# Performance work log

Hardware: AMD Instinct MI355X
Metric: run time of the kernel (lower is better)

## Reference

```python
import jax, jax.numpy as jnp
import numpy as np

DIM = 1024
H = 16
DH = DIM // H
LN_EPS = 1e-5


def _linear_params(key, din, dout):
    kw, kb = jax.random.split(key)
    bound = 1.0 / np.sqrt(din)
    W = jax.random.uniform(kw, (din, dout), jnp.float32, -bound, bound)
    b = jax.random.uniform(kb, (dout,), jnp.float32, -bound, bound)
    return W, b


def setup_inputs() -> dict:
    key = jax.random.key(0)
    ks = jax.random.split(key, 10)
    inp = {
        "Q": jax.random.normal(ks[0], (8, 512, DIM), jnp.float32),
        "K1": jax.random.normal(ks[1], (8, 1024, DIM), jnp.float32),
        "K2": jax.random.normal(ks[2], (8, 1024, DIM), jnp.float32),
    }
    for name, k in zip(["q", "k1", "k2", "v1", "v2", "o"], ks[3:9]):
        W, b = _linear_params(k, DIM, DIM)
        inp["W" + name] = W
        inp["b" + name] = b
    inp["g0"] = jnp.ones((DIM,), jnp.float32)
    inp["beta0"] = jnp.zeros((DIM,), jnp.float32)
    inp["g1"] = jnp.ones((DIM,), jnp.float32)
    inp["beta1"] = jnp.zeros((DIM,), jnp.float32)
    return inp


def _layernorm(x, g, b):
    m = jnp.mean(x, axis=-1, keepdims=True)
    v = jnp.mean(jnp.square(x - m), axis=-1, keepdims=True)
    return (x - m) * jax.lax.rsqrt(v + LN_EPS) * g + b


def _split_heads(x):
    # torch.cat(x.split(dh, 2), dim=0): [B,N,D] -> [H*B, N, dh], head-major on axis 0
    B, N, _ = x.shape
    return x.reshape(B, N, H, DH).transpose(2, 0, 1, 3).reshape(H * B, N, DH)


def _merge_heads(x, B):
    # inverse: torch.cat(out.split(B, 0), 2)
    _, N, _ = x.shape
    return x.reshape(H, B, N, DH).transpose(1, 2, 0, 3).reshape(B, N, DIM)


def reference(Q, K1, K2, Wq, bq, Wk1, bk1, Wk2, bk2, Wv1, bv1, Wv2, bv2, Wo, bo, g0, beta0, g1, beta1):
    B = Q.shape[0]
    Qp = Q @ Wq + bq
    # NOTE: faithful to source — V is computed from the ALREADY key-projected K_dict
    K1p = K1 @ Wk1 + bk1
    K2p = K2 @ Wk2 + bk2
    V1p = K1p @ Wv1 + bv1
    V2p = K2p @ Wv2 + bv2
    Q_ = _split_heads(Qp)                                   # [H*B, Nq, dh]
    K_ = jnp.concatenate([_split_heads(K1p), _split_heads(K2p)], axis=1)  # [H*B, Nk, dh]
    V_ = jnp.concatenate([_split_heads(V1p), _split_heads(V2p)], axis=1)
    scores = jnp.einsum("bqd,bkd->bqk", Q_, K_) / np.sqrt(DIM).astype(np.float32)
    # NOTE: faithful to source — softmax over the QUERY axis (dim=1)
    A = jax.nn.softmax(scores, axis=1)
    out = Q_ + jnp.einsum("bqk,bkd->bqd", A, V_)
    out = _merge_heads(out, B)                              # [B, Nq, DIM]
    out = _layernorm(out, g0, beta0)
    out = out + jax.nn.relu(out @ Wo + bo)
    out = _layernorm(out, g1, beta1)
    return out
```

## Files before the change

### kernel.cpp

```cpp
#include <hip/hip_runtime.h>
#include <math.h>

typedef __attribute__((ext_vector_type(8))) _Float16 half8v;
typedef __attribute__((ext_vector_type(4))) _Float16 half4v;
typedef __attribute__((ext_vector_type(4))) float f32x4;

__device__ __forceinline__ void gload16(const void* g, void* l) {
  __builtin_amdgcn_global_load_lds(
      (const __attribute__((address_space(1))) void*)g,
      (__attribute__((address_space(3))) void*)l, 16, 0, 0);
}

struct WP { const float* src; _Float16* dst; };
struct WPArgs { WP w[6]; };

__global__ __launch_bounds__(256)
void wprep_kernel(WPArgs args) {
  __shared__ float tile[32][33];
  const WP wp = args.w[blockIdx.z];
  const int t  = threadIdx.x;
  const int r  = t >> 3;
  const int c  = (t & 7) * 4;
  const int n0 = blockIdx.x * 32;
  const int k0 = blockIdx.y * 32;
  float4 v = *(const float4*)(wp.src + (size_t)(k0 + r) * 1024 + n0 + c);
  tile[r][c] = v.x; tile[r][c + 1] = v.y; tile[r][c + 2] = v.z; tile[r][c + 3] = v.w;
  __syncthreads();
  half4v h;
  #pragma unroll
  for (int i = 0; i < 4; ++i) h[i] = (_Float16)tile[c + i][r];
  *(half4v*)(wp.dst + (size_t)(n0 + r) * 1024 + k0 + c) = h;
}

__global__ __launch_bounds__(256)
void aconv_kernel(const float* __restrict__ in, _Float16* __restrict__ out, int n4) {
  int i = blockIdx.x * 256 + threadIdx.x;
  if (i >= n4) return;
  float4 v = ((const float4*)in)[i];
  half4v o;
  o[0] = (_Float16)v.x; o[1] = (_Float16)v.y; o[2] = (_Float16)v.z; o[3] = (_Float16)v.w;
  ((half4v*)out)[i] = o;
}

template<int MODE>
__global__ __launch_bounds__(256)
void gemm_fp16(const _Float16* __restrict__ A, const _Float16* __restrict__ B,
               const float* __restrict__ bias, const _Float16* __restrict__ X,
               _Float16* __restrict__ C, float* __restrict__ Cf,
               _Float16* __restrict__ Vt, int NM) {
  __shared__ _Float16 smem[16384];
  _Float16* const sA = smem;
  _Float16* const sB = smem + 8192;
  const int t    = threadIdx.x;
  const int bid  = blockIdx.x;
  const int xcd  = bid & 7;
  const int li   = bid >> 3;
  const int m    = xcd * (NM >> 3) + (li >> 3);
  const int n    = li & 7;
  const int bm   = m * 128;
  const int bn   = n * 128;
  const int lane = t & 63;
  const int w    = t >> 6;
  const int wr   = (w >> 1) * 64;
  const int wc   = (w & 1) * 64;
  const int lm   = lane & 15;
  const int lq   = lane >> 4;

  f32x4 acc[4][4];
  #pragma unroll
  for (int i = 0; i < 4; ++i)
    #pragma unroll
    for (int j = 0; j < 4; ++j) { f32x4 z = {0.f, 0.f, 0.f, 0.f}; acc[i][j] = z; }

  for (int k0 = 0; k0 < 1024; k0 += 64) {
    __syncthreads();
    #pragma unroll
    for (int i = 0; i < 4; ++i) {
      const int T    = w * 4 + i;
      const int kq   = T >> 1;
      const int row  = (T & 1) * 64 + lane;
      gload16(A + (size_t)(bm + row) * 1024 + k0 + kq * 8, &sA[(T * 64 + lane) * 8]);
      gload16(B + (size_t)(bn + row) * 1024 + k0 + kq * 8, &sB[(T * 64 + lane) * 8]);
    }
    __syncthreads();

    #pragma unroll
    for (int kk = 0; kk < 2; ++kk) {
      half8v af[4], bf[4];
      #pragma unroll
      for (int mi = 0; mi < 4; ++mi)
        af[mi] = *(const half8v*)&sA[((kk * 4 + lq) * 128 + wr + mi * 16 + lm) * 8];
      #pragma unroll
      for (int ni = 0; ni < 4; ++ni)
        bf[ni] = *(const half8v*)&sB[((kk * 4 + lq) * 128 + wc + ni * 16 + lm) * 8];
      #pragma unroll
      for (int mi = 0; mi < 4; ++mi)
        #pragma unroll
        for (int ni = 0; ni < 4; ++ni)
          acc[mi][ni] = __builtin_amdgcn_mfma_f32_16x16x32_f16(af[mi], bf[ni], acc[mi][ni], 0, 0, 0);
    }
  }

  float bv[4];
  #pragma unroll
  for (int ni = 0; ni < 4; ++ni) bv[ni] = bias[bn + wc + ni * 16 + lm];

  if (MODE == 1) {
    #pragma unroll
    for (int mi = 0; mi < 4; ++mi)
      #pragma unroll
      for (int ni = 0; ni < 4; ++ni) {
        const int col = bn + wc + ni * 16 + lm;
        #pragma unroll
        for (int j = 0; j < 4; ++j) {
          const int row = bm + wr + mi * 16 + lq * 4 + j;
          const size_t idx = (size_t)row * 1024 + col;
          Cf[idx] = (float)X[idx] + fmaxf(acc[mi][ni][j] + bv[ni], 0.f);
        }
      }
    return;
  }

  __syncthreads();
  #pragma unroll
  for (int mi = 0; mi < 4; ++mi)
    #pragma unroll
    for (int ni = 0; ni < 4; ++ni) {
      const int cc = wc + ni * 16 + lm;
      #pragma unroll
      for (int j = 0; j < 4; ++j) {
        const int rr = wr + mi * 16 + lq * 4 + j;
        const _Float16 v = (_Float16)(acc[mi][ni][j] + bv[ni]);
        if (MODE == 0) smem[rr * 128 + cc] = v;
        else           smem[cc * 128 + rr] = v;
      }
    }
  __syncthreads();
  const int r16 = t >> 4;
  const int c8  = (t & 15) * 8;
  #pragma unroll
  for (int p = 0; p < 8; ++p) {
    const int row = p * 16 + r16;
    half8v vv = *(const half8v*)&smem[row * 128 + c8];
    if (MODE == 0) *(half8v*)(C + (size_t)(bm + row) * 1024 + bn + c8) = vv;
    else           *(half8v*)(Vt + (size_t)(bn + row) * 8192 + bm + c8) = vv;
  }
}

__global__ __launch_bounds__(1024, 4)
void attn_mfma(const _Float16* __restrict__ Qp,
               const _Float16* __restrict__ K1p, const _Float16* __restrict__ K2p,
               const _Float16* __restrict__ VT1, const _Float16* __restrict__ VT2,
               float* __restrict__ Opart) {
  __shared__ _Float16 sK[2][2048];
  __shared__ _Float16 sV[2][2560];
  __shared__ _Float16 sP[20480];
  __shared__ float sZ[16][32];

  const int t    = threadIdx.x;
  const int lane = t & 63;
  const int w    = t >> 6;
  const int lm   = lane & 15;
  const int lq   = lane >> 4;
  const int hb   = blockIdx.x;
  const int ks   = blockIdx.y;
  const int h    = hb >> 3;
  const int b    = hb & 7;
  const int qw   = w * 32;
  const _Float16* __restrict__ K  = ks ? K2p : K1p;
  const _Float16* __restrict__ VT = ks ? VT2 : VT1;

  half8v qf[2][2];
  #pragma unroll
  for (int mi = 0; mi < 2; ++mi)
    #pragma unroll
    for (int dh = 0; dh < 2; ++dh)
      qf[mi][dh] = *(const half8v*)(Qp + (size_t)(b * 512 + qw + mi * 16 + lm) * 1024
                                       + h * 64 + dh * 32 + lq * 8);

  f32x4 o[2][4];
  #pragma unroll
  for (int i = 0; i < 2; ++i)
    #pragma unroll
    for (int j = 0; j < 4; ++j) { f32x4 z = {0.f, 0.f, 0.f, 0.f}; o[i][j] = z; }

  const int ku = t & 255;
  const int sd = ku & 31;
  const int sc = ku >> 5;
  const int vd = ku & 63;
  const int vc = (ku >> 6) & 3;
  _Float16* sPw = sP + w * 1280;

  half8v rk, rv;
  #define ISSUE_LOADS(K0)                                                                  \
    if (t < 256)      rk = *(const half8v*)(K + (size_t)(b * 1024 + (K0) + sd) * 1024 + h * 64 + sc * 8); \
    else if (t < 512) rv = *(const half8v*)(VT + (size_t)(h * 64 + vd) * 8192 + b * 1024 + (K0) + vc * 8);

  ISSUE_LOADS(0)

  for (int kt = 0; kt < 32; ++kt) {
    const int c = kt & 1;
    if (t < 256)      *(half8v*)&sK[c][(sc * 32 + sd) * 8] = rk;
    else if (t < 512) *(half8v*)&sV[c][vd * 40 + vc * 8] = rv;
    if (kt + 1 < 32) { ISSUE_LOADS((kt + 1) * 32) }
    __syncthreads();

    f32x4 s[2][2];
    #pragma unroll
    for (int i = 0; i < 2; ++i)
      #pragma unroll
      for (int j = 0; j < 2; ++j) { f32x4 z = {0.f, 0.f, 0.f, 0.f}; s[i][j] = z; }
    __builtin_amdgcn_s_setprio(1);
    #pragma unroll
    for (int dh = 0; dh < 2; ++dh) {
      half8v kb[2];
      #pragma unroll
      for (int fi = 0; fi < 2; ++fi)
        kb[fi] = *(const half8v*)&sK[c][((dh * 4 + lq) * 32 + fi * 16 + lm) * 8];
      #pragma unroll
      for (int mi = 0; mi < 2; ++mi)
        #pragma unroll
        for (int fi = 0; fi < 2; ++fi)
          s[mi][fi] = __builtin_amdgcn_mfma_f32_16x16x32_f16(qf[mi][dh], kb[fi], s[mi][fi], 0, 0, 0);
    }
    __builtin_amdgcn_s_setprio(0);

    float zp[2] = {0.f, 0.f};
    #pragma unroll
    for (int mi = 0; mi < 2; ++mi)
      #pragma unroll
      for (int fi = 0; fi < 2; ++fi)
        #pragma unroll
        for (int j = 0; j < 4; ++j) {
          float p = __expf(s[mi][fi][j] * 0.03125f);
          s[mi][fi][j] = p;
          zp[fi] += p;
        }
    #pragma unroll
    for (int fi = 0; fi < 2; ++fi) {
      zp[fi] += __shfl_xor(zp[fi], 16);
      zp[fi] += __shfl_xor(zp[fi], 32);
    }
    if (lane < 16) { sZ[w][lm] = zp[0]; sZ[w][16 + lm] = zp[1]; }
    __syncthreads();

    float iz = 0.f;
    if (lane < 32) {
      float z = 0.f;
      #pragma unroll
      for (int wv = 0; wv < 16; ++wv) z += sZ[wv][lane];
      iz = 1.0f / z;
    }
    const float iz0 = __shfl(iz, lm);
    const float iz1 = __shfl(iz, 16 + lm);

    #pragma unroll
    for (int mi = 0; mi < 2; ++mi)
      #pragma unroll
      for (int j = 0; j < 4; ++j) {
        const int q = mi * 16 + lq * 4 + j;
        sPw[q * 40 + lm]      = (_Float16)(s[mi][0][j] * iz0);
        sPw[q * 40 + 16 + lm] = (_Float16)(s[mi][1][j] * iz1);
      }

    half8v pa[2], vb[4];
    #pragma unroll
    for (int mi = 0; mi < 2; ++mi)
      pa[mi] = *(const half8v*)&sPw[(mi * 16 + lm) * 40 + lq * 8];
    #pragma unroll
    for (int ni = 0; ni < 4; ++ni)
      vb[ni] = *(const half8v*)&sV[c][(ni * 16 + lm) * 40 + lq * 8];
    __builtin_amdgcn_s_setprio(1);
    #pragma unroll
    for (int mi = 0; mi < 2; ++mi)
      #pragma unroll
      for (int ni = 0; ni < 4; ++ni)
        o[mi][ni] = __builtin_amdgcn_mfma_f32_16x16x32_f16(pa[mi], vb[ni], o[mi][ni], 0, 0, 0);
    __builtin_amdgcn_s_setprio(0);
  }
  #undef ISSUE_LOADS

  float* dst = Opart + (size_t)(ks * 128 + hb) * 512 * 64;
  #pragma unroll
  for (int mi = 0; mi < 2; ++mi)
    #pragma unroll
    for (int ni = 0; ni < 4; ++ni)
      #pragma unroll
      for (int j = 0; j < 4; ++j) {
        const int q = qw + mi * 16 + lq * 4 + j;
        const int d = ni * 16 + lm;
        dst[(size_t)q * 64 + d] = o[mi][ni][j];
      }
}

template<int MODE>
__global__ __launch_bounds__(256)
void ln_kernel(const float* __restrict__ fin, const _Float16* __restrict__ Qp,
               const float* __restrict__ g, const float* __restrict__ beta,
               _Float16* __restrict__ oh, float* __restrict__ of) {
  const int row = blockIdx.x;
  const int t = threadIdx.x;
  const int c = t * 4;
  float4 v;
  if (MODE == 0) {
    const int b  = row >> 9;
    const int n  = row & 511;
    const int hh = c >> 6;
    const int d  = c & 63;
    const int hb = hh * 8 + b;
    half4v qv = *(const half4v*)(Qp + (size_t)row * 1024 + c);
    float4 p0 = *(const float4*)&fin[((size_t)hb         * 512 + n) * 64 + d];
    float4 p1 = *(const float4*)&fin[((size_t)(128 + hb) * 512 + n) * 64 + d];
    v = make_float4((float)qv[0] + p0.x + p1.x, (float)qv[1] + p0.y + p1.y,
                    (float)qv[2] + p0.z + p1.z, (float)qv[3] + p0.w + p1.w);
  } else {
    v = *(const float4*)&fin[(size_t)row * 1024 + c];
  }
  float s  = v.x + v.y + v.z + v.w;
  float s2 = v.x * v.x + v.y * v.y + v.z * v.z + v.w * v.w;
  #pragma unroll
  for (int m = 1; m < 64; m <<= 1) { s += __shfl_xor(s, m); s2 += __shfl_xor(s2, m); }
  __shared__ float aS[4], aS2[4];
  const int wid = t >> 6;
  if ((t & 63) == 0) { aS[wid] = s; aS2[wid] = s2; }
  __syncthreads();
  s  = aS[0] + aS[1] + aS[2] + aS[3];
  s2 = aS2[0] + aS2[1] + aS2[2] + aS2[3];
  const float mean = s * (1.f / 1024.f);
  const float var  = s2 * (1.f / 1024.f) - mean * mean;
  const float rstd = rsqrtf(var + 1e-5f);
  float4 gg = *(const float4*)&g[c];
  float4 bb = *(const float4*)&beta[c];
  float4 ov = make_float4((v.x - mean) * rstd * gg.x + bb.x,
                          (v.y - mean) * rstd * gg.y + bb.y,
                          (v.z - mean) * rstd * gg.z + bb.z,
                          (v.w - mean) * rstd * gg.w + bb.w);
  const size_t oi = (size_t)row * 1024 + c;
  if (MODE == 0) {
    half4v hv;
    hv[0] = (_Float16)ov.x; hv[1] = (_Float16)ov.y;
    hv[2] = (_Float16)ov.z; hv[3] = (_Float16)ov.w;
    *(half4v*)(oh + oi) = hv;
  } else {
    *(float4*)(of + oi) = ov;
  }
}

extern "C" void kernel_launch(void* const* d_in, const int* in_sizes, int n_in,
                              void* d_out, int out_size, void* d_ws, size_t ws_size,
                              hipStream_t stream) {
  (void)in_sizes; (void)n_in; (void)out_size; (void)ws_size;
  const float* Q   = (const float*)d_in[0];
  const float* K1  = (const float*)d_in[1];
  const float* K2  = (const float*)d_in[2];
  const float* Wq  = (const float*)d_in[3];
  const float* bq  = (const float*)d_in[4];
  const float* Wk1 = (const float*)d_in[5];
  const float* bk1 = (const float*)d_in[6];
  const float* Wk2 = (const float*)d_in[7];
  const float* bk2 = (const float*)d_in[8];
  const float* Wv1 = (const float*)d_in[9];
  const float* bv1 = (const float*)d_in[10];
  const float* Wv2 = (const float*)d_in[11];
  const float* bv2 = (const float*)d_in[12];
  const float* Wo  = (const float*)d_in[13];
  const float* bo  = (const float*)d_in[14];
  const float* g0  = (const float*)d_in[15];
  const float* be0 = (const float*)d_in[16];
  const float* g1  = (const float*)d_in[17];
  const float* be1 = (const float*)d_in[18];

  char* WS = (char*)d_ws;
  const size_t MB = 1024 * 1024;
  auto S = [&](size_t off) { return (_Float16*)(WS + off); };
  _Float16 *Qc = S(0), *K1c = S(8 * MB), *K2c = S(24 * MB);
  _Float16 *Wt[6];
  for (int i = 0; i < 6; ++i) Wt[i] = S(40 * MB + i * 2 * MB);
  _Float16 *Qp  = S(52 * MB);
  _Float16 *K1p = S(60 * MB), *K2p = S(76 * MB);
  _Float16 *VT1 = S(92 * MB), *VT2 = S(108 * MB);
  float* Op = (float*)(WS + 124 * MB);
  _Float16 *x0 = S(0);
  float* tb = (float*)(WS + 8 * MB);

  WPArgs wa;
  const float* wsrc[6] = {Wq, Wk1, Wk2, Wv1, Wv2, Wo};
  for (int i = 0; i < 6; ++i) { wa.w[i].src = wsrc[i]; wa.w[i].dst = Wt[i]; }

  wprep_kernel<<<dim3(32, 32, 6), 256, 0, stream>>>(wa);
  aconv_kernel<<<dim3(4096), 256, 0, stream>>>(Q,  Qc,  1048576);
  aconv_kernel<<<dim3(8192), 256, 0, stream>>>(K1, K1c, 2097152);
  aconv_kernel<<<dim3(8192), 256, 0, stream>>>(K2, K2c, 2097152);

  gemm_fp16<0><<<dim3(256), 256, 0, stream>>>(Qc,  Wt[0], bq,  nullptr, Qp,  nullptr, nullptr, 32);
  gemm_fp16<0><<<dim3(512), 256, 0, stream>>>(K1c, Wt[1], bk1, nullptr, K1p, nullptr, nullptr, 64);
  gemm_fp16<0><<<dim3(512), 256, 0, stream>>>(K2c, Wt[2], bk2, nullptr, K2p, nullptr, nullptr, 64);
  gemm_fp16<2><<<dim3(512), 256, 0, stream>>>(K1p, Wt[3], bv1, nullptr, nullptr, nullptr, VT1, 64);
  gemm_fp16<2><<<dim3(512), 256, 0, stream>>>(K2p, Wt[4], bv2, nullptr, nullptr, nullptr, VT2, 64);

  attn_mfma<<<dim3(128, 2), dim3(1024), 0, stream>>>(Qp, K1p, K2p, VT1, VT2, Op);

  ln_kernel<0><<<dim3(4096), 256, 0, stream>>>(Op, Qp, g0, be0, x0, nullptr);
  gemm_fp16<1><<<dim3(256), 256, 0, stream>>>(x0, Wt[5], bo, x0, nullptr, tb, nullptr, 32);
  ln_kernel<1><<<dim3(4096), 256, 0, stream>>>(tb, nullptr, g1, be1, nullptr, (float*)d_out);
}
```

Measured before the change: 488.7 us.

## Compose key and value weights so K and V projections share one GEMM

```diff
diff --git a/kernel.cpp b/kernel.cpp
--- a/kernel.cpp
+++ b/kernel.cpp
@@ -42,12 +42,26 @@
   ((half4v*)out)[i] = o;
 }
 
+__global__ __launch_bounds__(256)
+void bias_compose(const float* __restrict__ bk, const float* __restrict__ bv,
+                  const _Float16* __restrict__ Wvt, float* __restrict__ out) {
+  const int n = blockIdx.x * 256 + threadIdx.x;
+  const _Float16* row = Wvt + (size_t)n * 1024;
+  float s = bv[n];
+  for (int k = 0; k < 1024; k += 8) {
+    half8v wv = *(const half8v*)&row[k];
+    #pragma unroll
+    for (int j = 0; j < 8; ++j) s += bk[k + j] * (float)wv[j];
+  }
+  out[n] = s;
+}
+
 template<int MODE>
 __global__ __launch_bounds__(256)
 void gemm_fp16(const _Float16* __restrict__ A, const _Float16* __restrict__ B,
                const float* __restrict__ bias, const _Float16* __restrict__ X,
                _Float16* __restrict__ C, float* __restrict__ Cf,
-               _Float16* __restrict__ Vt, int NM) {
+               _Float16* __restrict__ Vt, int NM, int NN, int ostride) {
   __shared__ _Float16 smem[16384];
   _Float16* const sA = smem;
   _Float16* const sB = smem + 8192;
@@ -55,8 +69,8 @@
   const int bid  = blockIdx.x;
   const int xcd  = bid & 7;
   const int li   = bid >> 3;
-  const int m    = xcd * (NM >> 3) + (li >> 3);
-  const int n    = li & 7;
+  const int m    = xcd * (NM >> 3) + li / NN;
+  const int n    = li % NN;
   const int bm   = m * 128;
   const int bn   = n * 128;
   const int lane = t & 63;
@@ -121,6 +135,7 @@
     return;
   }
 
+  const bool tr = (MODE == 2) || (MODE == 3 && bn >= 1024);
   __syncthreads();
   #pragma unroll
   for (int mi = 0; mi < 4; ++mi)
@@ -131,8 +146,8 @@
       for (int j = 0; j < 4; ++j) {
         const int rr = wr + mi * 16 + lq * 4 + j;
         const _Float16 v = (_Float16)(acc[mi][ni][j] + bv[ni]);
-        if (MODE == 0) smem[rr * 128 + cc] = v;
-        else           smem[cc * 128 + rr] = v;
+        if (!tr) smem[rr * 128 + cc] = v;
+        else     smem[cc * 128 + rr] = v;
       }
     }
   __syncthreads();
@@ -142,8 +157,12 @@
   for (int p = 0; p < 8; ++p) {
     const int row = p * 16 + r16;
     half8v vv = *(const half8v*)&smem[row * 128 + c8];
-    if (MODE == 0) *(half8v*)(C + (size_t)(bm + row) * 1024 + bn + c8) = vv;
-    else           *(half8v*)(Vt + (size_t)(bn + row) * 8192 + bm + c8) = vv;
+    if (!tr) {
+      *(half8v*)(C + (size_t)(bm + row) * 1024 + bn + c8) = vv;
+    } else {
+      const int nb = (MODE == 3) ? (bn - 1024) : bn;
+      *(half8v*)(Vt + (size_t)(nb + row) * ostride + bm + c8) = vv;
+    }
   }
 }
 
@@ -376,31 +395,47 @@
   _Float16 *Qc = S(0), *K1c = S(8 * MB), *K2c = S(24 * MB);
   _Float16 *Wt[6];
   for (int i = 0; i < 6; ++i) Wt[i] = S(40 * MB + i * 2 * MB);
-  _Float16 *Qp  = S(52 * MB);
-  _Float16 *K1p = S(60 * MB), *K2p = S(76 * MB);
-  _Float16 *VT1 = S(92 * MB), *VT2 = S(108 * MB);
-  float* Op = (float*)(WS + 124 * MB);
+  _Float16 *Wk1c = S(52 * MB), *Wk2c = S(54 * MB);
+  _Float16 *Wc1 = S(56 * MB), *Wc2 = S(60 * MB);
+  float *bc1 = (float*)(WS + 64 * MB);
+  float *bc2 = (float*)(WS + 64 * MB + 8 * 1024);
+  float *zb  = (float*)(WS + 64 * MB + 16 * 1024);
+  _Float16 *Qp  = S(65 * MB);
+  _Float16 *K1p = S(73 * MB), *K2p = S(89 * MB);
+  _Float16 *VT1 = S(105 * MB), *VT2 = S(121 * MB);
+  float* Op = (float*)(WS + 137 * MB);
   _Float16 *x0 = S(0);
   float* tb = (float*)(WS + 8 * MB);
 
   WPArgs wa;
   const float* wsrc[6] = {Wq, Wk1, Wk2, Wv1, Wv2, Wo};
-  for (int i = 0; i < 6; ++i) { wa.w[i].src = wsrc[i]; wa.w[i].dst = Wt[i]; }
+  _Float16* wdst[6] = {Wt[0], Wc1 , Wc2 , Wt[3], Wt[4], Wt[5]};
+  for (int i = 0; i < 6; ++i) { wa.w[i].src = wsrc[i]; wa.w[i].dst = wdst[i]; }
 
   wprep_kernel<<<dim3(32, 32, 6), 256, 0, stream>>>(wa);
-  aconv_kernel<<<dim3(4096), 256, 0, stream>>>(Q,  Qc,  1048576);
-  aconv_kernel<<<dim3(8192), 256, 0, stream>>>(K1, K1c, 2097152);
-  aconv_kernel<<<dim3(8192), 256, 0, stream>>>(K2, K2c, 2097152);
-
-  gemm_fp16<0><<<dim3(256), 256, 0, stream>>>(Qc,  Wt[0], bq,  nullptr, Qp,  nullptr, nullptr, 32);
-  gemm_fp16<0><<<dim3(512), 256, 0, stream>>>(K1c, Wt[1], bk1, nullptr, K1p, nullptr, nullptr, 64);
-  gemm_fp16<0><<<dim3(512), 256, 0, stream>>>(K2c, Wt[2], bk2, nullptr, K2p, nullptr, nullptr, 64);
-  gemm_fp16<2><<<dim3(512), 256, 0, stream>>>(K1p, Wt[3], bv1, nullptr, nullptr, nullptr, VT1, 64);
-  gemm_fp16<2><<<dim3(512), 256, 0, stream>>>(K2p, Wt[4], bv2, nullptr, nullptr, nullptr, VT2, 64);
+  aconv_kernel<<<dim3(4096), 256, 0, stream>>>(Q,   Qc,   1048576);
+  aconv_kernel<<<dim3(8192), 256, 0, stream>>>(K1,  K1c,  2097152);
+  aconv_kernel<<<dim3(8192), 256, 0, stream>>>(K2,  K2c,  2097152);
+  aconv_kernel<<<dim3(1024), 256, 0, stream>>>(Wk1, Wk1c, 262144);
+  aconv_kernel<<<dim3(1024), 256, 0, stream>>>(Wk2, Wk2c, 262144);
+  hipMemsetAsync(zb, 0, 4096, stream);
+  hipMemcpyAsync(bc1, bk1, 4096, hipMemcpyDeviceToDevice, stream);
+  hipMemcpyAsync(bc2, bk2, 4096, hipMemcpyDeviceToDevice, stream);
+  bias_compose<<<dim3(4), 256, 0, stream>>>(bk1, bv1, Wt[3], bc1 + 1024);
+  bias_compose<<<dim3(4), 256, 0, stream>>>(bk2, bv2, Wt[4], bc2 + 1024);
+
+  gemm_fp16<2><<<dim3(64), 256, 0, stream>>>(Wk1c, Wt[3], zb, nullptr,
+                                             nullptr, nullptr, Wc1 + (size_t)1024 * 1024, 8, 8, 1024);
+  gemm_fp16<2><<<dim3(64), 256, 0, stream>>>(Wk2c, Wt[4], zb, nullptr,
+                                             nullptr, nullptr, Wc2 + (size_t)1024 * 1024, 8, 8, 1024);
+
+  gemm_fp16<0><<<dim3(256),  256, 0, stream>>>(Qc,  Wt[0], bq, nullptr, Qp, nullptr, nullptr, 32, 8, 0);
+  gemm_fp16<3><<<dim3(1024), 256, 0, stream>>>(K1c, Wc1, bc1, nullptr, K1p, nullptr, VT1, 64, 16, 8192);
+  gemm_fp16<3><<<dim3(1024), 256, 0, stream>>>(K2c, Wc2, bc2, nullptr, K2p, nullptr, VT2, 64, 16, 8192);
 
   attn_mfma<<<dim3(128, 2), dim3(1024), 0, stream>>>(Qp, K1p, K2p, VT1, VT2, Op);
 
   ln_kernel<0><<<dim3(4096), 256, 0, stream>>>(Op, Qp, g0, be0, x0, nullptr);
-  gemm_fp16<1><<<dim3(256), 256, 0, stream>>>(x0, Wt[5], bo, x0, nullptr, tb, nullptr, 32);
+  gemm_fp16<1><<<dim3(256), 256, 0, stream>>>(x0, Wt[5], bo, x0, nullptr, tb, nullptr, 32, 8, 0);
   ln_kernel<1><<<dim3(4096), 256, 0, stream>>>(tb, nullptr, g1, be1, nullptr, (float*)d_out);
 }
```

Result: slower. 609.8 us (+24.8%).
